# Optimization experiments

Measured on AMD Instinct MI355X. Metric: run time of the kernel, lower is better.

Reference implementation:

```python
import jax, jax.numpy as jnp
import numpy as np
import math

B, N_TOK, C, H = 8, 1024, 384, 6
K, S, P = 3, 2, 1
OUT_C, HID = 384, 4 * 384
EPS = 1e-5
NEG_INF = float('-inf')


def _build_conv_mask(num_token, k, s, p):
    """Replicates ConvAttentionMask (include_cls_token=True). Returns (mask[(N+2),(N+2)], idx[(W,k^2)] with -1 for padding)."""
    I = int(math.sqrt(num_token))
    ref = np.arange(num_token).reshape(I, I)
    ref = np.pad(ref, ((0, p), (0, p)), constant_values=-1)
    cent = np.arange(k // 2 - p, I - k // 2 + p, s)
    cc = np.stack(np.meshgrid(cent, cent, indexing='ij'), -1).reshape(-1, 1, 2)  # cartesian_prod order
    ke = np.arange(-(k // 2), k // 2 + 1)
    kc = np.stack(np.meshgrid(ke, ke, indexing='ij'), -1).reshape(1, -1, 2)
    coords = cc + kc  # (W, k^2, 2); negative coords wrap like torch fancy indexing -> hit -1 padding
    idx = ref[coords[..., 0], coords[..., 1]]  # (W, k^2)
    mask = np.full((num_token, num_token), NEG_INF, np.float32)
    for w in idx:
        v = w[w >= 0]
        mask[np.ix_(v, v)] = 1.0
    idx = idx + (idx >= 0).astype(np.int32)  # shift for cls token; -1 stays -1
    mask = np.pad(mask, ((1, 0), (1, 0)), constant_values=1.0)  # cls row/col
    mask = np.pad(mask, ((0, 1), (0, 1)), constant_values=0.0)  # extra zero-padded token
    return mask, idx

MASK_NP, IDX_NP = _build_conv_mask(N_TOK, K, S, P)
W_WIN = IDX_NP.shape[0]
# torch negative index -1 on a length-(N_TOK+1) tensor -> wrap to last token
IDX_FLAT = np.where(IDX_NP < 0, IDX_NP + N_TOK + 1, IDX_NP).reshape(-1)


def _ln(x, w, b):
    mu = jnp.mean(x, -1, keepdims=True)
    var = jnp.mean(jnp.square(x - mu), -1, keepdims=True)
    return (x - mu) * jax.lax.rsqrt(var + EPS) * w + b


def setup_inputs() -> dict:
    key = jax.random.key(0)
    ks = jax.random.split(key, 8)
    sd = 0.02
    return {
        'x': jax.random.normal(ks[0], (B, N_TOK + 1, C), jnp.float32),
        'norm1_w': jnp.ones((C,), jnp.float32), 'norm1_b': jnp.zeros((C,), jnp.float32),
        'qkv_w': sd * jax.random.normal(ks[1], (3 * C, C), jnp.float32),
        'proj_w': sd * jax.random.normal(ks[2], (C, C), jnp.float32),
        'proj_b': jnp.zeros((C,), jnp.float32),
        'norm2_w': jnp.ones((C,), jnp.float32), 'norm2_b': jnp.zeros((C,), jnp.float32),
        'pool_w': sd * jax.random.normal(ks[3], (C, K * K * C), jnp.float32),
        'pool_b': jnp.zeros((C,), jnp.float32),
        'norm3_w': jnp.ones((C,), jnp.float32), 'norm3_b': jnp.zeros((C,), jnp.float32),
        'fc1_w': sd * jax.random.normal(ks[4], (HID, C), jnp.float32),
        'fc1_b': jnp.zeros((HID,), jnp.float32),
        'fc2_w': sd * jax.random.normal(ks[5], (OUT_C, HID), jnp.float32),
        'fc2_b': jnp.zeros((OUT_C,), jnp.float32),
    }


def reference(x, norm1_w, norm1_b, qkv_w, proj_w, proj_b, norm2_w, norm2_b,
              pool_w, pool_b, norm3_w, norm3_b, fc1_w, fc1_b, fc2_w, fc2_b):
    mask = jnp.asarray(MASK_NP)  # (N_TOK+2, N_TOK+2), values in {-inf, 0, 1}
    Bv, N, Cv = x.shape
    d = Cv // H
    h = _ln(x, norm1_w, norm1_b)
    h = jnp.pad(h, ((0, 0), (0, 1), (0, 0)))  # append zero token -> (B, N+1, C)
    M = N + 1
    # attention (scale = num_heads**-0.5 as in the source, qkv has no bias)
    qkv = (h @ qkv_w.T).reshape(Bv, M, 3, H, d).transpose(2, 0, 3, 1, 4)
    q, k, v = qkv[0], qkv[1], qkv[2]
    scores = jnp.einsum('bhqd,bhkd->bhqk', q, k) * (H ** -0.5)
    # multiplicative mask {-inf,0,1}: keep where 1, zero where 0, -inf where -inf (intended semantics)
    scores = jnp.where(mask == 1.0, scores, jnp.where(mask == 0.0, 0.0, NEG_INF))
    probs = jax.nn.softmax(scores, axis=-1)
    attn = jnp.einsum('bhqk,bhkd->bhqd', probs, v).transpose(0, 2, 1, 3).reshape(Bv, M, Cv)
    attn = attn @ proj_w.T + proj_b
    h = h + attn
    h = h[:, :-1, :]  # drop padded token -> (B, N, C)
    h = _ln(h, norm2_w, norm2_b)
    # conv-style pooling: gather k^2 tokens per window, project
    gathered = h[:, IDX_FLAT, :].reshape(Bv, W_WIN, K * K * Cv)
    tok = gathered @ pool_w.T + pool_b  # (B, W, C)
    h = jnp.concatenate([h[:, :1, :], tok], axis=1)  # prepend cls -> (B, W+1, C)
    h = _ln(h, norm3_w, norm3_b)
    h = jax.nn.gelu(h @ fc1_w.T + fc1_b, approximate=False)
    return h @ fc2_w.T + fc2_b  # (B, W+1, OUT_C)
```

## Files before the change

### kernel.cpp

```cpp
#include <hip/hip_runtime.h>


typedef unsigned short u16;
typedef unsigned int u32;
typedef short s16x8 __attribute__((ext_vector_type(8)));
typedef float f32x4 __attribute__((ext_vector_type(4)));

__device__ __forceinline__ float b2f(u16 u) {
    return __uint_as_float(((u32)u) << 16);
}
__device__ __forceinline__ u16 f2b(float f) {
    u32 u = __float_as_uint(f);
    return (u16)((u + 0x7FFFu + ((u >> 16) & 1u)) >> 16);
}
__device__ __forceinline__ float wave_sum(float v) {
#pragma unroll
    for (int o = 32; o > 0; o >>= 1) v += __shfl_xor(v, o, 64);
    return v;
}
__device__ __forceinline__ float wave_max(float v) {
#pragma unroll
    for (int o = 32; o > 0; o >>= 1) v = fmaxf(v, __shfl_xor(v, o, 64));
    return v;
}
__device__ __forceinline__ float half_sum(float v) {
#pragma unroll
    for (int o = 16; o > 0; o >>= 1) v += __shfl_xor(v, o, 64);
    return v;
}
__device__ __forceinline__ float half_max(float v) {
#pragma unroll
    for (int o = 16; o > 0; o >>= 1) v = fmaxf(v, __shfl_xor(v, o, 64));
    return v;
}
__device__ __forceinline__ float dot8(const float* qsh, int d0, uint4 u) {
    return qsh[d0 + 0] * b2f((u16)(u.x)) + qsh[d0 + 1] * b2f((u16)(u.x >> 16)) +
           qsh[d0 + 2] * b2f((u16)(u.y)) + qsh[d0 + 3] * b2f((u16)(u.y >> 16)) +
           qsh[d0 + 4] * b2f((u16)(u.z)) + qsh[d0 + 5] * b2f((u16)(u.z >> 16)) +
           qsh[d0 + 6] * b2f((u16)(u.w)) + qsh[d0 + 7] * b2f((u16)(u.w >> 16));
}

#define CCH 384
#define SCALE 0.40824829046386302f
#define NEG_BIG (-1e30f)

#define W_QKV 0
#define W_PROJ 442368
#define W_POOL 589824
#define W_FC1 1916928
#define W_FC2 2506752
#define W_TOTAL 3096576

__device__ __forceinline__ void ln_from_f32(const float* in, const float* w,
                                            const float* bb, u16* out,
                                            int lane) {
    float v[6];
    float s = 0.f, ss = 0.f;
#pragma unroll
    for (int i = 0; i < 6; i++) {
        v[i] = in[lane + 64 * i];
        s += v[i];
        ss += v[i] * v[i];
    }
    s = wave_sum(s);
    ss = wave_sum(ss);
    float mu = s * (1.f / 384.f);
    float var = ss * (1.f / 384.f) - mu * mu;
    float inv = rsqrtf(var + 1e-5f);
#pragma unroll
    for (int i = 0; i < 6; i++) {
        int c = lane + 64 * i;
        out[c] = f2b((v[i] - mu) * inv * w[c] + bb[c]);
    }
}
__device__ __forceinline__ void ln_from_b16(const u16* in, const float* w,
                                            const float* bb, u16* out,
                                            int lane) {
    float v[6];
    float s = 0.f, ss = 0.f;
#pragma unroll
    for (int i = 0; i < 6; i++) {
        v[i] = b2f(in[lane + 64 * i]);
        s += v[i];
        ss += v[i] * v[i];
    }
    s = wave_sum(s);
    ss = wave_sum(ss);
    float mu = s * (1.f / 384.f);
    float var = ss * (1.f / 384.f) - mu * mu;
    float inv = rsqrtf(var + 1e-5f);
#pragma unroll
    for (int i = 0; i < 6; i++) {
        int c = lane + 64 * i;
        out[c] = f2b((v[i] - mu) * inv * w[c] + bb[c]);
    }
}

#define PRO_LN 2052
#define PRO_CVT 1512
#define PRO_ZERO 771
__global__ __launch_bounds__(256) void prologue(
    const float* __restrict__ x, const float* __restrict__ n1w,
    const float* __restrict__ n1b, u16* __restrict__ h1,
    const float* __restrict__ qkv_w, const float* __restrict__ proj_w,
    const float* __restrict__ pool_w, const float* __restrict__ fc1_w,
    const float* __restrict__ fc2_w, u16* __restrict__ wb,
    float* __restrict__ dout) {
    int bid = blockIdx.x, tid = threadIdx.x;
    if (bid < PRO_LN) {
        int wv = tid >> 6, lane = tid & 63;
        int row = bid * 4 + wv;
        int t = row % 1026, b = row / 1026;
        u16* out = h1 + (size_t)row * CCH;
        if (t == 1025) {
#pragma unroll
            for (int i = 0; i < 6; i++) out[lane + 64 * i] = 0;
            return;
        }
        ln_from_f32(x + ((size_t)b * 1025 + t) * CCH, n1w, n1b, out, lane);
    } else if (bid < PRO_LN + PRO_CVT) {
        size_t off = ((size_t)(bid - PRO_LN) * 256 + tid) * 8;
        if (off >= W_TOTAL) return;
        const float* src;
        size_t base;
        if (off < W_PROJ)       { src = qkv_w;  base = W_QKV; }
        else if (off < W_POOL)  { src = proj_w; base = W_PROJ; }
        else if (off < W_FC1)   { src = pool_w; base = W_POOL; }
        else if (off < W_FC2)   { src = fc1_w;  base = W_FC1; }
        else                    { src = fc2_w;  base = W_FC2; }
        size_t rel = off - base;
        float4 a = *(const float4*)(src + rel);
        float4 b = *(const float4*)(src + rel + 4);
        uint4 o;
        o.x = (u32)f2b(a.x) | ((u32)f2b(a.y) << 16);
        o.y = (u32)f2b(a.z) | ((u32)f2b(a.w) << 16);
        o.z = (u32)f2b(b.x) | ((u32)f2b(b.y) << 16);
        o.w = (u32)f2b(b.z) | ((u32)f2b(b.w) << 16);
        *(uint4*)(wb + off) = o;
    } else {
        size_t idx = ((size_t)(bid - PRO_LN - PRO_CVT) * 256 + tid) * 4;
        *(float4*)(dout + idx) = make_float4(0.f, 0.f, 0.f, 0.f);
    }
}

#define MID_LN 2050
#define MID_ZERO 768
__global__ __launch_bounds__(256) void midk(u16* __restrict__ h,
                                            const float* __restrict__ n2w,
                                            const float* __restrict__ n2b,
                                            float* __restrict__ tokf) {
    int bid = blockIdx.x, tid = threadIdx.x;
    if (bid < MID_LN) {
        int wv = tid >> 6, lane = tid & 63;
        int row = bid * 4 + wv;
        int b = row / 1025, t = row % 1025;
        u16* p = h + ((size_t)b * 1026 + t) * CCH;
        ln_from_b16(p, n2w, n2b, p, lane);
    } else {
        size_t idx = ((size_t)(bid - MID_LN) * 256 + tid) * 4;
        *(float4*)(tokf + idx) = make_float4(0.f, 0.f, 0.f, 0.f);
    }
}

__global__ __launch_bounds__(64) void ln3_concat(const u16* __restrict__ h2,
                                                 const float* __restrict__ tokf,
                                                 const float* __restrict__ w,
                                                 const float* __restrict__ bb,
                                                 u16* __restrict__ h3) {
    int row = blockIdx.x;
    int b = row / 257, t = row % 257;
    int lane = threadIdx.x;
    u16* out = h3 + (size_t)row * CCH;
    if (t == 0) {
        ln_from_b16(h2 + (size_t)b * 1026 * CCH, w, bb, out, lane);
    } else {
        ln_from_f32(tokf + ((size_t)b * 256 + (t - 1)) * CCH, w, bb, out, lane);
    }
}

template <int TN, bool GATHER, int SPLITK, bool BIAS, bool GELU_ACT, bool RES,
          bool ATOMIC>
__global__ __launch_bounds__(256) void gemm_mf(const u16* __restrict__ A,
                                               int lda,
                                               const u16* __restrict__ Bwb,
                                               const float* __restrict__ bias,
                                               const u16* __restrict__ Res,
                                               void* __restrict__ Yv, int M,
                                               int N, int K) {
    __shared__ u16 Asl[128 * 40];
    __shared__ u16 Bsl[TN * 40];
    const int tid = threadIdx.x;
    const int wave = tid >> 6, lane = tid & 63;
    const int quad = lane >> 4, l15 = lane & 15;
    const int m0 = blockIdx.y * 128, n0 = blockIdx.x * TN;
    const int kp = (SPLITK > 1) ? blockIdx.z : 0;
    const int KS = K / SPLITK;
    const int kbase = kp * KS;

    f32x4 acc[2][TN / 16];
#pragma unroll
    for (int i = 0; i < 2; i++)
#pragma unroll
        for (int j = 0; j < TN / 16; j++) acc[i][j] = (f32x4){0.f, 0.f, 0.f, 0.f};

    for (int kt = 0; kt < KS; kt += 32) {
        const int kk = kbase + kt;
#pragma unroll
        for (int L = 0; L < 2; L++) {
            int linear = L * 256 + tid;
            int row = linear >> 2, seg = linear & 3;
            int kf = kk + seg * 8;
            const u16* src;
            if (GATHER) {
                int m = m0 + row;
                int b = m >> 8, w = m & 255;
                int j = kf / 384, rem = kf - j * 384;
                int pr = 2 * (w >> 4) + j / 3 - 1;
                int pc = 2 * (w & 15) + j % 3 - 1;
                int tok = (pr >= 0 && pr < 32 && pc >= 0 && pc < 32)
                              ? (32 * pr + pc + 1)
                              : 1024;
                src = A + ((size_t)b * 1026 + tok) * 384 + rem;
            } else {
                int m = m0 + row;
                if (m >= M) m = M - 1;
                src = A + (size_t)m * lda + kf;
            }
            *(uint4*)(&Asl[row * 40 + seg * 8]) = *(const uint4*)src;
        }
#pragma unroll
        for (int L = 0; L < TN / 64; L++) {
            int linear = L * 256 + tid;
            int row = linear >> 2, seg = linear & 3;
            *(uint4*)(&Bsl[row * 40 + seg * 8]) =
                *(const uint4*)(Bwb + (size_t)(n0 + row) * K + kk + seg * 8);
        }
        __syncthreads();
        s16x8 afr[2], bfr[TN / 16];
#pragma unroll
        for (int ms = 0; ms < 2; ms++)
            afr[ms] = *(const s16x8*)(&Asl[(wave * 32 + ms * 16 + l15) * 40 +
                                           quad * 8]);
#pragma unroll
        for (int ns = 0; ns < TN / 16; ns++)
            bfr[ns] = *(const s16x8*)(&Bsl[(ns * 16 + l15) * 40 + quad * 8]);
#pragma unroll
        for (int ms = 0; ms < 2; ms++)
#pragma unroll
            for (int ns = 0; ns < TN / 16; ns++)
                acc[ms][ns] = __builtin_amdgcn_mfma_f32_16x16x32_bf16(
                    afr[ms], bfr[ns], acc[ms][ns], 0, 0, 0);
        __syncthreads();
    }
#pragma unroll
    for (int ms = 0; ms < 2; ms++) {
#pragma unroll
        for (int ns = 0; ns < TN / 16; ns++) {
            int n = n0 + ns * 16 + l15;
#pragma unroll
            for (int i = 0; i < 4; i++) {
                int m = m0 + wave * 32 + ms * 16 + quad * 4 + i;
                if (m >= M) continue;
                float v = acc[ms][ns][i];
                if (BIAS && (SPLITK == 1 || kp == 0)) v += bias[n];
                if (RES) v += b2f(Res[(size_t)m * N + n]);
                if (GELU_ACT) v = 0.5f * v * (1.f + erff(v * 0.70710678118f));
                if (ATOMIC)
                    atomicAdd((float*)Yv + (size_t)m * N + n, v);
                else
                    ((u16*)Yv)[(size_t)m * N + n] = f2b(v);
            }
        }
    }
}

__global__ __launch_bounds__(64) void attn_patch(u16* __restrict__ qkv) {
    int bid = blockIdx.x;
    int idx = bid & 511;
    int hb = bid >> 9;
    int h = hb % 6, b = hb / 6;
    int lane = threadIdx.x;
    int hl = lane >> 5, l5 = lane & 31;
    int p0 = idx * 2;
    int p = p0 | hl;
    int r = p >> 5, c = p & 31;
    int rlo, rhi, clo, chi;
    if (r & 1) { rlo = (r - 2 < 0) ? 0 : r - 2; rhi = (r + 2 > 31) ? 31 : r + 2; }
    else       { rlo = (r - 1 < 0) ? 0 : r - 1; rhi = (r + 1 > 31) ? 31 : r + 1; }
    if (c & 1) { clo = (c - 2 < 0) ? 0 : c - 2; chi = (c + 2 > 31) ? 31 : c + 2; }
    else       { clo = (c - 1 < 0) ? 0 : c - 1; chi = (c + 1 > 31) ? 31 : c + 1; }
    int nr = rhi - rlo + 1, nc = chi - clo + 1;
    int nk = nr * nc + 1;
    int tok = 0;
    if (l5 >= 1 && l5 < nk) {
        int jj = l5 - 1;
        tok = 1 + ((rlo + jj / nc) << 5) + (clo + jj % nc);
    }
    u16* base = qkv + (size_t)b * 1026 * 1152 + h * 64;
    __shared__ float qsh[2][64];
    qsh[0][lane] = b2f(base[(size_t)(1 + p0) * 1152 + lane]);
    qsh[1][lane] = b2f(base[(size_t)(2 + p0) * 1152 + lane]);
    __syncthreads();
    float sc = NEG_BIG;
    if (l5 < nk) {
        const u16* krow = base + (size_t)tok * 1152 + 384;
        float acc = 0.f;
#pragma unroll
        for (int d0 = 0; d0 < 64; d0 += 8)
            acc += dot8(qsh[hl], d0, *(const uint4*)(krow + d0));
        sc = acc * SCALE;
    }
    float mx = fmaxf(half_max(sc), 0.f);
    float pe = (l5 < nk) ? expf(sc - mx) : 0.f;
    float Z = half_sum(pe) + expf(-mx);
    float o0 = 0.f, o1 = 0.f;
#pragma unroll
    for (int j = 0; j < 26; j++) {
        int t = __shfl(tok, (hl << 5) | j, 64);
        float wj = __shfl(pe, (hl << 5) | j, 64);
        u32 vv = *(const u32*)(base + (size_t)t * 1152 + 768 + 2 * l5);
        o0 += wj * b2f((u16)vv);
        o1 += wj * b2f((u16)(vv >> 16));
    }
    float zi = 1.f / Z;
    u32 packed = (u32)f2b(o0 * zi) | ((u32)f2b(o1 * zi) << 16);
    *(u32*)(base + (size_t)(1 + p) * 1152 + 2 * l5) = packed;
}

__global__ __launch_bounds__(1024) void attn_cls(u16* __restrict__ qkv) {
    int h = blockIdx.x % 6, b = blockIdx.x / 6;
    u16* base = qkv + (size_t)b * 1026 * 1152 + h * 64;
    int tid = threadIdx.x, lane = tid & 63, wv = tid >> 6;
    __shared__ float sc[1026];
    __shared__ float qsh[64];
    __shared__ float redmax[16], redsum[16];
    __shared__ float pv[16][64];
    if (tid < 64) qsh[tid] = b2f(base[tid]);
    __syncthreads();
    for (int key = tid; key < 1026; key += 1024) {
        const u16* krow = base + (size_t)key * 1152 + 384;
        float acc = 0.f;
#pragma unroll
        for (int d0 = 0; d0 < 64; d0 += 8)
            acc += dot8(qsh, d0, *(const uint4*)(krow + d0));
        sc[key] = acc * SCALE;
    }
    __syncthreads();
    float lm = NEG_BIG;
    for (int key = tid; key < 1026; key += 1024) lm = fmaxf(lm, sc[key]);
    lm = wave_max(lm);
    if (lane == 0) redmax[wv] = lm;
    __syncthreads();
    float mx = NEG_BIG;
#pragma unroll
    for (int i = 0; i < 16; i++) mx = fmaxf(mx, redmax[i]);
    float lsum = 0.f;
    for (int key = tid; key < 1026; key += 1024) {
        float e = expf(sc[key] - mx);
        sc[key] = e;
        lsum += e;
    }
    lsum = wave_sum(lsum);
    if (lane == 0) redsum[wv] = lsum;
    __syncthreads();
    float Z = 0.f;
#pragma unroll
    for (int i = 0; i < 16; i++) Z += redsum[i];
    float acc = 0.f;
#pragma unroll
    for (int t = 0; t < 65; t++) {
        int key = wv + 16 * t;
        bool ok = key < 1026;
        int kc = ok ? key : 1025;
        float p = ok ? sc[kc] : 0.f;
        acc += p * b2f(base[(size_t)kc * 1152 + 768 + lane]);
    }
    pv[wv][lane] = acc;
    __syncthreads();
    if (tid < 64) {
        float s = 0.f;
#pragma unroll
        for (int w2 = 0; w2 < 16; w2++) s += pv[w2][tid];
        base[tid] = f2b(s / Z);
        base[(size_t)1025 * 1152 + tid] = 0;
    }
}

extern "C" void kernel_launch(void* const* d_in, const int* in_sizes, int n_in,
                              void* d_out, int out_size, void* d_ws,
                              size_t ws_size, hipStream_t stream) {
    const float* x      = (const float*)d_in[0];
    const float* n1w    = (const float*)d_in[1];
    const float* n1b    = (const float*)d_in[2];
    const float* qkv_w  = (const float*)d_in[3];
    const float* proj_w = (const float*)d_in[4];
    const float* proj_b = (const float*)d_in[5];
    const float* n2w    = (const float*)d_in[6];
    const float* n2b    = (const float*)d_in[7];
    const float* pool_w = (const float*)d_in[8];
    const float* pool_b = (const float*)d_in[9];
    const float* n3w    = (const float*)d_in[10];
    const float* n3b    = (const float*)d_in[11];
    const float* fc1_w  = (const float*)d_in[12];
    const float* fc1_b  = (const float*)d_in[13];
    const float* fc2_w  = (const float*)d_in[14];
    const float* fc2_b  = (const float*)d_in[15];

    u16* ws = (u16*)d_ws;
    u16* h1    = ws;
    u16* qkvb  = ws + 3151872;
    u16* wb    = ws + 12607488;
    float* tokf = (float*)qkvb;
    u16* h3    = qkvb + 1572864;
    u16* mlp1  = qkvb + 2362368;

    prologue<<<PRO_LN + PRO_CVT + PRO_ZERO, 256, 0, stream>>>(
        x, n1w, n1b, h1, qkv_w, proj_w, pool_w, fc1_w, fc2_w, wb,
        (float*)d_out);
    gemm_mf<128, false, 1, false, false, false, false>
        <<<dim3(1152 / 128, 65), 256, 0, stream>>>(h1, 384, wb + W_QKV,
                                                   nullptr, nullptr, qkvb,
                                                   8208, 1152, 384);
    attn_patch<<<8 * 6 * 512, 64, 0, stream>>>(qkvb);
    attn_cls<<<8 * 6, 1024, 0, stream>>>(qkvb);
    gemm_mf<64, false, 1, true, false, true, false>
        <<<dim3(384 / 64, 65), 256, 0, stream>>>(qkvb, 1152, wb + W_PROJ,
                                                 proj_b, h1, h1, 8208, 384,
                                                 384);
    midk<<<MID_LN + MID_ZERO, 256, 0, stream>>>(h1, n2w, n2b, tokf);
    gemm_mf<64, true, 4, true, false, false, true>
        <<<dim3(384 / 64, 16, 4), 256, 0, stream>>>(h1, 384, wb + W_POOL,
                                                    pool_b, nullptr, tokf,
                                                    2048, 384, 3456);
    ln3_concat<<<8 * 257, 64, 0, stream>>>(h1, tokf, n3w, n3b, h3);
    gemm_mf<64, false, 1, true, true, false, false>
        <<<dim3(1536 / 64, 17), 256, 0, stream>>>(h3, 384, wb + W_FC1, fc1_b,
                                                  nullptr, mlp1, 2056, 1536,
                                                  384);
    gemm_mf<64, false, 4, true, false, false, true>
        <<<dim3(384 / 64, 17, 4), 256, 0, stream>>>(mlp1, 1536, wb + W_FC2,
                                                    fc2_b, nullptr, d_out,
                                                    2056, 384, 1536);
}
```

Before: 274.1 us.

## Use direct global-to-LDS loads with XOR swizzle in GEMM; merge attention kernels

```diff
diff --git a/kernel.cpp b/kernel.cpp
--- a/kernel.cpp
+++ b/kernel.cpp
@@ -12,6 +12,11 @@
 __device__ __forceinline__ u16 f2b(float f) {
     u32 u = __float_as_uint(f);
     return (u16)((u + 0x7FFFu + ((u >> 16) & 1u)) >> 16);
+}
+__device__ __forceinline__ void gload16(const void* g, void* l) {
+    __builtin_amdgcn_global_load_lds(
+        (const __attribute__((address_space(1))) void*)g,
+        (__attribute__((address_space(3))) void*)l, 16, 0, 0);
 }
 __device__ __forceinline__ float wave_sum(float v) {
 #pragma unroll
@@ -187,15 +192,18 @@
                                                const u16* __restrict__ Res,
                                                void* __restrict__ Yv, int M,
                                                int N, int K) {
-    __shared__ u16 Asl[128 * 40];
-    __shared__ u16 Bsl[TN * 40];
+    __shared__ u16 Asl[128 * 32];
+    __shared__ u16 Bsl[TN * 32];
     const int tid = threadIdx.x;
     const int wave = tid >> 6, lane = tid & 63;
     const int quad = lane >> 4, l15 = lane & 15;
+    const int wvu = __builtin_amdgcn_readfirstlane(wave);
     const int m0 = blockIdx.y * 128, n0 = blockIdx.x * TN;
     const int kp = (SPLITK > 1) ? blockIdx.z : 0;
     const int KS = K / SPLITK;
     const int kbase = kp * KS;
+    const int srow = tid >> 2;
+    const int sseg = (tid & 3) ^ (srow & 3);
 
     f32x4 acc[2][TN / 16];
 #pragma unroll
@@ -205,11 +213,10 @@
 
     for (int kt = 0; kt < KS; kt += 32) {
         const int kk = kbase + kt;
+        const int kf = kk + sseg * 8;
 #pragma unroll
         for (int L = 0; L < 2; L++) {
-            int linear = L * 256 + tid;
-            int row = linear >> 2, seg = linear & 3;
-            int kf = kk + seg * 8;
+            int row = L * 64 + srow;
             const u16* src;
             if (GATHER) {
                 int m = m0 + row;
@@ -226,24 +233,24 @@
                 if (m >= M) m = M - 1;
                 src = A + (size_t)m * lda + kf;
             }
-            *(uint4*)(&Asl[row * 40 + seg * 8]) = *(const uint4*)src;
+            gload16(src, &Asl[(size_t)(L * 256 + wvu * 64) * 8]);
         }
 #pragma unroll
         for (int L = 0; L < TN / 64; L++) {
-            int linear = L * 256 + tid;
-            int row = linear >> 2, seg = linear & 3;
-            *(uint4*)(&Bsl[row * 40 + seg * 8]) =
-                *(const uint4*)(Bwb + (size_t)(n0 + row) * K + kk + seg * 8);
+            int row = L * 64 + srow;
+            gload16(Bwb + (size_t)(n0 + row) * K + kf,
+                    &Bsl[(size_t)(L * 256 + wvu * 64) * 8]);
         }
         __syncthreads();
         s16x8 afr[2], bfr[TN / 16];
+        const int rslot = (quad ^ (l15 & 3)) * 8;
 #pragma unroll
         for (int ms = 0; ms < 2; ms++)
-            afr[ms] = *(const s16x8*)(&Asl[(wave * 32 + ms * 16 + l15) * 40 +
-                                           quad * 8]);
+            afr[ms] =
+                *(const s16x8*)(&Asl[(wave * 32 + ms * 16 + l15) * 32 + rslot]);
 #pragma unroll
         for (int ns = 0; ns < TN / 16; ns++)
-            bfr[ns] = *(const s16x8*)(&Bsl[(ns * 16 + l15) * 40 + quad * 8]);
+            bfr[ns] = *(const s16x8*)(&Bsl[(ns * 16 + l15) * 32 + rslot]);
 #pragma unroll
         for (int ms = 0; ms < 2; ms++)
 #pragma unroll
@@ -274,12 +281,61 @@
     }
 }
 
-__global__ __launch_bounds__(64) void attn_patch(u16* __restrict__ qkv) {
+__global__ __launch_bounds__(64) void attn_win(u16* __restrict__ qkv) {
     int bid = blockIdx.x;
-    int idx = bid & 511;
-    int hb = bid >> 9;
+    int lane = threadIdx.x;
+    __shared__ float sc[1026];
+    __shared__ float qsh[2][64];
+    if (bid < 48) {
+        int h = bid % 6, b = bid / 6;
+        u16* base = qkv + (size_t)b * 1026 * 1152 + h * 64;
+        float* qs = &qsh[0][0];
+        qs[lane] = b2f(base[lane]);
+        __syncthreads();
+        float lm = NEG_BIG;
+#pragma unroll
+        for (int t = 0; t < 17; t++) {
+            int key = lane + 64 * t;
+            if (key < 1026) {
+                const u16* krow = base + (size_t)key * 1152 + 384;
+                float acc = 0.f;
+#pragma unroll
+                for (int d0 = 0; d0 < 64; d0 += 8)
+                    acc += dot8(qs, d0, *(const uint4*)(krow + d0));
+                float s = acc * SCALE;
+                sc[key] = s;
+                lm = fmaxf(lm, s);
+            }
+        }
+        float mx = wave_max(lm);
+        float ls = 0.f;
+#pragma unroll
+        for (int t = 0; t < 17; t++) {
+            int key = lane + 64 * t;
+            if (key < 1026) {
+                float e = expf(sc[key] - mx);
+                sc[key] = e;
+                ls += e;
+            }
+        }
+        float Z = wave_sum(ls);
+        __syncthreads();
+        float oa = 0.f, ob = 0.f;
+#pragma unroll 4
+        for (int k2 = 0; k2 < 513; k2++) {
+            oa += sc[2 * k2] * b2f(base[(size_t)(2 * k2) * 1152 + 768 + lane]);
+            ob += sc[2 * k2 + 1] *
+                  b2f(base[(size_t)(2 * k2 + 1) * 1152 + 768 + lane]);
+        }
+        float o = (oa + ob) / Z;
+        base[lane] = f2b(o);
+        base[(size_t)1025 * 1152 + lane] = 0;
+        return;
+    }
+    int pbid = bid - 48;
+    int idx = pbid & 511;
+    int hb = pbid >> 9;
     int h = hb % 6, b = hb / 6;
-    int lane = threadIdx.x;
     int hl = lane >> 5, l5 = lane & 31;
     int p0 = idx * 2;
     int p = p0 | hl;
@@ -297,21 +353,20 @@
         tok = 1 + ((rlo + jj / nc) << 5) + (clo + jj % nc);
     }
     u16* base = qkv + (size_t)b * 1026 * 1152 + h * 64;
-    __shared__ float qsh[2][64];
     qsh[0][lane] = b2f(base[(size_t)(1 + p0) * 1152 + lane]);
     qsh[1][lane] = b2f(base[(size_t)(2 + p0) * 1152 + lane]);
     __syncthreads();
-    float sc = NEG_BIG;
+    float scp = NEG_BIG;
     if (l5 < nk) {
         const u16* krow = base + (size_t)tok * 1152 + 384;
         float acc = 0.f;
 #pragma unroll
         for (int d0 = 0; d0 < 64; d0 += 8)
             acc += dot8(qsh[hl], d0, *(const uint4*)(krow + d0));
-        sc = acc * SCALE;
-    }
-    float mx = fmaxf(half_max(sc), 0.f);
-    float pe = (l5 < nk) ? expf(sc - mx) : 0.f;
+        scp = acc * SCALE;
+    }
+    float mx = fmaxf(half_max(scp), 0.f);
+    float pe = (l5 < nk) ? expf(scp - mx) : 0.f;
     float Z = half_sum(pe) + expf(-mx);
     float o0 = 0.f, o1 = 0.f;
 #pragma unroll
@@ -325,65 +380,6 @@
     float zi = 1.f / Z;
     u32 packed = (u32)f2b(o0 * zi) | ((u32)f2b(o1 * zi) << 16);
     *(u32*)(base + (size_t)(1 + p) * 1152 + 2 * l5) = packed;
-}
-
-__global__ __launch_bounds__(1024) void attn_cls(u16* __restrict__ qkv) {
-    int h = blockIdx.x % 6, b = blockIdx.x / 6;
-    u16* base = qkv + (size_t)b * 1026 * 1152 + h * 64;
-    int tid = threadIdx.x, lane = tid & 63, wv = tid >> 6;
-    __shared__ float sc[1026];
-    __shared__ float qsh[64];
-    __shared__ float redmax[16], redsum[16];
-    __shared__ float pv[16][64];
-    if (tid < 64) qsh[tid] = b2f(base[tid]);
-    __syncthreads();
-    for (int key = tid; key < 1026; key += 1024) {
-        const u16* krow = base + (size_t)key * 1152 + 384;
-        float acc = 0.f;
-#pragma unroll
-        for (int d0 = 0; d0 < 64; d0 += 8)
-            acc += dot8(qsh, d0, *(const uint4*)(krow + d0));
-        sc[key] = acc * SCALE;
-    }
-    __syncthreads();
-    float lm = NEG_BIG;
-    for (int key = tid; key < 1026; key += 1024) lm = fmaxf(lm, sc[key]);
-    lm = wave_max(lm);
-    if (lane == 0) redmax[wv] = lm;
-    __syncthreads();
-    float mx = NEG_BIG;
-#pragma unroll
-    for (int i = 0; i < 16; i++) mx = fmaxf(mx, redmax[i]);
-    float lsum = 0.f;
-    for (int key = tid; key < 1026; key += 1024) {
-        float e = expf(sc[key] - mx);
-        sc[key] = e;
-        lsum += e;
-    }
-    lsum = wave_sum(lsum);
-    if (lane == 0) redsum[wv] = lsum;
-    __syncthreads();
-    float Z = 0.f;
-#pragma unroll
-    for (int i = 0; i < 16; i++) Z += redsum[i];
-    float acc = 0.f;
-#pragma unroll
-    for (int t = 0; t < 65; t++) {
-        int key = wv + 16 * t;
-        bool ok = key < 1026;
-        int kc = ok ? key : 1025;
-        float p = ok ? sc[kc] : 0.f;
-        acc += p * b2f(base[(size_t)kc * 1152 + 768 + lane]);
-    }
-    pv[wv][lane] = acc;
-    __syncthreads();
-    if (tid < 64) {
-        float s = 0.f;
-#pragma unroll
-        for (int w2 = 0; w2 < 16; w2++) s += pv[w2][tid];
-        base[tid] = f2b(s / Z);
-        base[(size_t)1025 * 1152 + tid] = 0;
-    }
 }
 
 extern "C" void kernel_launch(void* const* d_in, const int* in_sizes, int n_in,
@@ -421,8 +417,7 @@
         <<<dim3(1152 / 128, 65), 256, 0, stream>>>(h1, 384, wb + W_QKV,
                                                    nullptr, nullptr, qkvb,
                                                    8208, 1152, 384);
-    attn_patch<<<8 * 6 * 512, 64, 0, stream>>>(qkvb);
-    attn_cls<<<8 * 6, 1024, 0, stream>>>(qkvb);
+    attn_win<<<48 + 8 * 6 * 512, 64, 0, stream>>>(qkvb);
     gemm_mf<64, false, 1, true, false, true, false>
         <<<dim3(384 / 64, 65), 256, 0, stream>>>(qkvb, 1152, wb + W_PROJ,
                                                  proj_b, h1, h1, 8208, 384,
```

Measured after the change: 315.9 us. +15.2%, slower.
